# Kernel tuning notes

Hardware: AMD Instinct MI355X
Metric: run time of the kernel (lower is better)

## Reference

```python
import jax, jax.numpy as jnp
import numpy as np

NEG_SLOPE = 0.01  # torch F.leaky_relu default


def _mlp_block(x, mask, W, b):
    # x: [B,P,V,F]; mask: [B,P,V] bool; W: [H,F]; b: [H]
    h = jax.nn.leaky_relu(jnp.einsum('bpvf,hf->bpvh', x, W) + b, NEG_SLOPE)
    m = mask[..., None]
    out = jnp.where(m, h, 0.0)                                   # zeros at masked-out slots
    neg = jnp.where(m, out, -jnp.inf)
    pool = jnp.max(neg, axis=2, keepdims=True)                   # [B,P,1,H] masked max-pool
    any_valid = jnp.any(mask, axis=2)[:, :, None, None]
    pool = jnp.where(any_valid, pool, 0.0)                       # fully-masked polylines -> 0
    rep = jnp.broadcast_to(pool, out.shape)
    return jnp.concatenate([out, rep], axis=-1)                  # [B,P,V,2H]


def setup_inputs() -> dict:
    key = jax.random.key(0)
    ks = jax.random.split(key, 8)
    B, P, V, F, H = 32, 512, 32, 16, 64
    input_var = jax.random.normal(ks[0], (B, P, V, F), dtype=jnp.float32)
    input_mask = jax.random.bernoulli(ks[1], 0.8, (B, P, V))
    s = 1.0 / np.sqrt(F)
    W1 = jax.random.uniform(ks[2], (H, F), jnp.float32, -s, s)
    b1 = jax.random.uniform(ks[3], (H,), jnp.float32, -s, s)
    s2 = 1.0 / np.sqrt(2 * H)
    W2 = jax.random.uniform(ks[4], (H, 2 * H), jnp.float32, -s2, s2)
    b2 = jax.random.uniform(ks[5], (H,), jnp.float32, -s2, s2)
    W3 = jax.random.uniform(ks[6], (H, 2 * H), jnp.float32, -s2, s2)
    b3 = jax.random.uniform(ks[7], (H,), jnp.float32, -s2, s2)
    return {"input_var": input_var, "input_mask": input_mask,
            "W1": W1, "b1": b1, "W2": W2, "b2": b2, "W3": W3, "b3": b3,
            "size1": P, "size2": V}


def reference(input_var, input_mask, W1, b1, W2, b2, W3, b3, size1, size2):
    hidden = W1.shape[0]
    x = _mlp_block(input_var, input_mask, W1, b1)
    y = _mlp_block(x, input_mask, W2, b2)
    z = _mlp_block(y, input_mask, W3, b3)
    out = z[:, :, 0, -hidden:]                                   # pooled half, same across V
    out = jnp.where(jnp.any(input_mask, axis=2)[..., None], out, 0.0)
    return out
```

## Files before the change

### kernel.cpp

```cpp
#include <hip/hip_runtime.h>
#include <math.h>

namespace {
constexpr int kXS = 72;
constexpr float kSlope = 0.01f;

typedef short bf16x8 __attribute__((ext_vector_type(8)));
typedef float f32x4  __attribute__((ext_vector_type(4)));

__device__ __forceinline__ float lrelu(float x) { return fmaxf(x, kSlope * x); }

__device__ __forceinline__ unsigned short bfrne(float a) {
    union { float f; unsigned u; } v; v.f = a;
    return (unsigned short)((v.u + 0x7FFFu + ((v.u >> 16) & 1u)) >> 16);
}

__device__ __forceinline__ unsigned cvtpk(float lo, float hi) {
    unsigned r;
    asm("v_cvt_pk_bf16_f32 %0, %1, %2" : "=v"(r) : "v"(lo), "v"(hi));
    return r;
}

__global__ void prep_weights(const float* __restrict__ W1,
                             const float* __restrict__ W2,
                             const float* __restrict__ W3,
                             unsigned short* __restrict__ ws)
{
    int t = blockIdx.x * blockDim.x + threadIdx.x;
    if (t >= 36 * 64) return;
    int f = t >> 6, l = t & 63, c = l & 15, q = l >> 4;
    unsigned short v[8] = {0, 0, 0, 0, 0, 0, 0, 0};
    const float* src = nullptr; int row = 0, k0 = 0, K = 0;
    if (f < 4) {
        if (q < 2) { src = W1; row = 16 * f + c; k0 = q * 8; K = 16; }
    } else if (f < 20) {
        int g = f - 4;  src = W2; row = 16 * (g >> 2) + c; k0 = (g & 3) * 32 + q * 8; K = 128;
    } else {
        int g = f - 20; src = W3; row = 16 * (g >> 2) + c; k0 = (g & 3) * 32 + q * 8; K = 128;
    }
    if (src) {
        #pragma unroll
        for (int j = 0; j < 8; ++j) v[j] = bfrne(src[row * K + k0 + j]);
    }
    unsigned short* dst = ws + (size_t)f * 512 + l * 8;
    *(ushort4*)(dst)     = make_ushort4(v[0], v[1], v[2], v[3]);
    *(ushort4*)(dst + 4) = make_ushort4(v[4], v[5], v[6], v[7]);
}

__global__ __launch_bounds__(256, 3) void fused_mlp_v8(
    const float* __restrict__ X, const int* __restrict__ M,
    const unsigned short* __restrict__ WF,
    const float* __restrict__ B1, const float* __restrict__ B2,
    const float* __restrict__ B3, float* __restrict__ OUT)
{
    __shared__ __align__(16) short sX[4][2][32 * kXS];
    __shared__ __align__(16) short sP[4][2][64];

    const int t = threadIdx.x, w = t >> 6, l = t & 63, c = l & 15, q = l >> 4;
    const size_t bp0 = (size_t)blockIdx.x * 8 + w * 2;

    unsigned mbits[2];
    bool anyv[2];
    #pragma unroll
    for (int u = 0; u < 2; ++u) {
        const int4* Mp = (const int4*)(M + (bp0 + u) * 32);
        const int4 mr0 = Mp[q], mr1 = Mp[4 + q];
        mbits[u] =
            (mr0.x ? 1u : 0u)  | (mr0.y ? 2u : 0u)  | (mr0.z ? 4u : 0u)  | (mr0.w ? 8u : 0u) |
            (mr1.x ? 16u : 0u) | (mr1.y ? 32u : 0u) | (mr1.z ? 64u : 0u) | (mr1.w ? 128u : 0u);
        anyv[u] = __any(mbits[u] != 0);
    }
    float addm[2][8];
    #pragma unroll
    for (int u = 0; u < 2; ++u)
        #pragma unroll
        for (int i = 0; i < 8; ++i)
            addm[u][i] = ((mbits[u] >> i) & 1u) ? 0.f : -INFINITY;

    bf16x8 a1f[2][2];
    #pragma unroll
    for (int u = 0; u < 2; ++u)
        #pragma unroll
        for (int mt = 0; mt < 2; ++mt) {
            union { bf16x8 v; unsigned uu[4]; } cv; cv.v = bf16x8{};
            if (q < 2) {
                const float4* p = (const float4*)(X + ((bp0 + u) * 32 + 16 * mt + c) * 16 + q * 8);
                float4 f0 = p[0], f1 = p[1];
                cv.uu[0] = cvtpk(f0.x, f0.y);
                cv.uu[1] = cvtpk(f0.z, f0.w);
                cv.uu[2] = cvtpk(f1.x, f1.y);
                cv.uu[3] = cvtpk(f1.z, f1.w);
            }
            a1f[u][mt] = cv.v;
        }

    f32x4 acc[2][2][4];

    #pragma unroll
    for (int nt = 0; nt < 4; ++nt) {
        float b1 = B1[16 * nt + c];
        bf16x8 wf = *(const bf16x8*)(WF + (size_t)nt * 512 + l * 8);
        f32x4 c0 = { b1, b1, b1, b1 };
        #pragma unroll
        for (int u = 0; u < 2; ++u) {
            acc[u][0][nt] = __builtin_amdgcn_mfma_f32_16x16x32_bf16(a1f[u][0], wf, c0, 0, 0, 0);
            acc[u][1][nt] = __builtin_amdgcn_mfma_f32_16x16x32_bf16(a1f[u][1], wf, c0, 0, 0, 0);
        }
    }

    auto epilogue = [&](int u, short* xb_, short* pl_) {
        float pool[4];
        #pragma unroll
        for (int nt = 0; nt < 4; ++nt) {
            float pv = -INFINITY;
            #pragma unroll
            for (int mt = 0; mt < 2; ++mt) {
                short* base = &xb_[(16 * mt + 4 * q) * kXS + 16 * nt + c];
                float y0 = lrelu(acc[u][mt][nt][0]);
                float y1 = lrelu(acc[u][mt][nt][1]);
                float y2 = lrelu(acc[u][mt][nt][2]);
                float y3 = lrelu(acc[u][mt][nt][3]);
                pv = fmaxf(pv, y0 + addm[u][mt * 4 + 0]);
                pv = fmaxf(pv, y1 + addm[u][mt * 4 + 1]);
                pv = fmaxf(pv, y2 + addm[u][mt * 4 + 2]);
                pv = fmaxf(pv, y3 + addm[u][mt * 4 + 3]);
                unsigned u01 = cvtpk(y0, y1);
                unsigned u23 = cvtpk(y2, y3);
                base[0 * kXS] = (short)u01;
                base[1 * kXS] = (short)(u01 >> 16);
                base[2 * kXS] = (short)u23;
                base[3 * kXS] = (short)(u23 >> 16);
            }
            pv = fmaxf(pv, __shfl_xor(pv, 16));
            pv = fmaxf(pv, __shfl_xor(pv, 32));
            pool[nt] = anyv[u] ? pv : 0.f;
        }
        float ps = (q & 2) ? ((q & 1) ? pool[3] : pool[2])
                           : ((q & 1) ? pool[1] : pool[0]);
        pl_[16 * q + c] = (short)cvtpk(ps, ps);
    };

    auto layerK = [&](int fb, const float* Bp) {
        #pragma unroll
        for (int nt = 0; nt < 4; ++nt) {
            float bb = Bp[16 * nt + c];
            #pragma unroll
            for (int u = 0; u < 2; ++u) {
                acc[u][0][nt] = f32x4{ bb, bb, bb, bb };
                acc[u][1][nt] = acc[u][0][nt];
            }
        }
        #pragma unroll
        for (int ks = 0; ks < 4; ++ks) {
            bf16x8 am[2][2];
            #pragma unroll
            for (int u = 0; u < 2; ++u) {
                const short* xb_ = &sX[w][u][0];
                const short* pl_ = &sP[w][u][0];
                if (ks < 2) {
                    am[u][0] = *(const bf16x8*)&xb_[(     c) * kXS + ks * 32 + q * 8];
                    am[u][1] = *(const bf16x8*)&xb_[(16 + c) * kXS + ks * 32 + q * 8];
                } else {
                    am[u][0] = *(const bf16x8*)&pl_[(ks - 2) * 32 + q * 8];
                    am[u][1] = am[u][0];
                }
            }
            #pragma unroll
            for (int nt = 0; nt < 4; ++nt) {
                bf16x8 wf = *(const bf16x8*)(WF + ((size_t)(fb + nt * 4 + ks)) * 512 + l * 8);
                #pragma unroll
                for (int u = 0; u < 2; ++u) {
                    acc[u][0][nt] = __builtin_amdgcn_mfma_f32_16x16x32_bf16(am[u][0], wf, acc[u][0][nt], 0, 0, 0);
                    acc[u][1][nt] = __builtin_amdgcn_mfma_f32_16x16x32_bf16(am[u][1], wf, acc[u][1][nt], 0, 0, 0);
                }
            }
        }
    };

    epilogue(0, &sX[w][0][0], &sP[w][0][0]);
    epilogue(1, &sX[w][1][0], &sP[w][1][0]);
    layerK(4, B2);

    epilogue(0, &sX[w][0][0], &sP[w][0][0]);
    epilogue(1, &sX[w][1][0], &sP[w][1][0]);
    layerK(20, B3);

    #pragma unroll
    for (int u = 0; u < 2; ++u) {
        float pool[4];
        #pragma unroll
        for (int nt = 0; nt < 4; ++nt) {
            float pv = -INFINITY;
            #pragma unroll
            for (int mt = 0; mt < 2; ++mt)
                #pragma unroll
                for (int r = 0; r < 4; ++r)
                    pv = fmaxf(pv, lrelu(acc[u][mt][nt][r]) + addm[u][mt * 4 + r]);
            pv = fmaxf(pv, __shfl_xor(pv, 16));
            pv = fmaxf(pv, __shfl_xor(pv, 32));
            pool[nt] = anyv[u] ? pv : 0.f;
        }
        float ps = (q & 2) ? ((q & 1) ? pool[3] : pool[2])
                           : ((q & 1) ? pool[1] : pool[0]);
        OUT[(bp0 + u) * 64 + 16 * q + c] = ps;
    }
}
}

extern "C" void kernel_launch(void* const* d_in, const int* in_sizes, int n_in,
                              void* d_out, int out_size, void* d_ws, size_t ws_size,
                              hipStream_t stream) {
    (void)in_sizes; (void)n_in; (void)ws_size; (void)out_size;
    const float* X  = (const float*)d_in[0];
    const int*   M  = (const int*)d_in[1];
    const float* W1 = (const float*)d_in[2];
    const float* B1 = (const float*)d_in[3];
    const float* W2 = (const float*)d_in[4];
    const float* B2 = (const float*)d_in[5];
    const float* W3 = (const float*)d_in[6];
    const float* B3 = (const float*)d_in[7];
    float* OUT = (float*)d_out;
    unsigned short* WF = (unsigned short*)d_ws;

    prep_weights<<<(36 * 64 + 255) / 256, 256, 0, stream>>>(W1, W2, W3, WF);
    fused_mlp_v8<<<2048, 256, 0, stream>>>(X, M, WF, B1, B2, B3, OUT);
}
```

Before: 122.7 us.

## Stage weights in LDS, prepack mask bits and biases, roll layer loops

```diff
diff --git a/kernel.cpp b/kernel.cpp
--- a/kernel.cpp
+++ b/kernel.cpp
@@ -21,61 +21,86 @@
     return r;
 }
 
-__global__ void prep_weights(const float* __restrict__ W1,
-                             const float* __restrict__ W2,
-                             const float* __restrict__ W3,
-                             unsigned short* __restrict__ ws)
+__global__ void prep_pack(const float* __restrict__ W1,
+                          const float* __restrict__ W2,
+                          const float* __restrict__ W3,
+                          const float* __restrict__ B1,
+                          const float* __restrict__ B2,
+                          const float* __restrict__ B3,
+                          const int* __restrict__ M,
+                          unsigned short* __restrict__ wsW,
+                          float* __restrict__ wsB,
+                          unsigned* __restrict__ wsM)
 {
     int t = blockIdx.x * blockDim.x + threadIdx.x;
-    if (t >= 36 * 64) return;
-    int f = t >> 6, l = t & 63, c = l & 15, q = l >> 4;
-    unsigned short v[8] = {0, 0, 0, 0, 0, 0, 0, 0};
-    const float* src = nullptr; int row = 0, k0 = 0, K = 0;
-    if (f < 4) {
-        if (q < 2) { src = W1; row = 16 * f + c; k0 = q * 8; K = 16; }
-    } else if (f < 20) {
-        int g = f - 4;  src = W2; row = 16 * (g >> 2) + c; k0 = (g & 3) * 32 + q * 8; K = 128;
-    } else {
-        int g = f - 20; src = W3; row = 16 * (g >> 2) + c; k0 = (g & 3) * 32 + q * 8; K = 128;
-    }
-    if (src) {
-        #pragma unroll
-        for (int j = 0; j < 8; ++j) v[j] = bfrne(src[row * K + k0 + j]);
-    }
-    unsigned short* dst = ws + (size_t)f * 512 + l * 8;
-    *(ushort4*)(dst)     = make_ushort4(v[0], v[1], v[2], v[3]);
-    *(ushort4*)(dst + 4) = make_ushort4(v[4], v[5], v[6], v[7]);
-}
-
-__global__ __launch_bounds__(256, 3) void fused_mlp_v8(
-    const float* __restrict__ X, const int* __restrict__ M,
-    const unsigned short* __restrict__ WF,
-    const float* __restrict__ B1, const float* __restrict__ B2,
-    const float* __restrict__ B3, float* __restrict__ OUT)
+    if (t < 36 * 64) {
+        int f = t >> 6, l = t & 63, c = l & 15, q = l >> 4;
+        unsigned short v[8] = {0, 0, 0, 0, 0, 0, 0, 0};
+        const float* src = nullptr; int row = 0, k0 = 0, K = 0;
+        if (f < 4) {
+            if (q < 2) { src = W1; row = 16 * f + c; k0 = q * 8; K = 16; }
+        } else if (f < 20) {
+            int g = f - 4;  src = W2; row = 16 * (g >> 2) + c; k0 = (g & 3) * 32 + q * 8; K = 128;
+        } else {
+            int g = f - 20; src = W3; row = 16 * (g >> 2) + c; k0 = (g & 3) * 32 + q * 8; K = 128;
+        }
+        if (src) {
+            #pragma unroll
+            for (int j = 0; j < 8; ++j) v[j] = bfrne(src[row * K + k0 + j]);
+        }
+        unsigned short* dst = wsW + (size_t)f * 512 + l * 8;
+        *(ushort4*)(dst)     = make_ushort4(v[0], v[1], v[2], v[3]);
+        *(ushort4*)(dst + 4) = make_ushort4(v[4], v[5], v[6], v[7]);
+    } else if (t < 36 * 64 + 192) {
+        int i = t - 36 * 64; int layer = i >> 6, j = i & 63;
+        const float* B = (layer == 0) ? B1 : (layer == 1) ? B2 : B3;
+        wsB[layer * 64 + (j & 15) * 4 + (j >> 4)] = B[j];
+    } else if (t < 36 * 64 + 192 + 16384) {
+        int bp = t - (36 * 64 + 192);
+        const int4* mp = (const int4*)(M + bp * 32);
+        unsigned bits = 0;
+        #pragma unroll
+        for (int i = 0; i < 8; ++i) {
+            int4 v = mp[i];
+            unsigned b = (v.x ? 1u : 0u) | (v.y ? 2u : 0u) |
+                         (v.z ? 4u : 0u) | (v.w ? 8u : 0u);
+            bits |= b << (4 * i);
+        }
+        wsM[bp] = bits;
+    }
+}
+
+__global__ __launch_bounds__(256, 3) void fused_mlp_v9(
+    const float* __restrict__ X, const unsigned* __restrict__ MPK,
+    const unsigned short* __restrict__ WFg, const float* __restrict__ BT,
+    float* __restrict__ OUT)
 {
+    __shared__ __align__(16) short sWF[36 * 512];
     __shared__ __align__(16) short sX[4][2][32 * kXS];
     __shared__ __align__(16) short sP[4][2][64];
 
     const int t = threadIdx.x, w = t >> 6, l = t & 63, c = l & 15, q = l >> 4;
     const size_t bp0 = (size_t)blockIdx.x * 8 + w * 2;
 
-    unsigned mbits[2];
+    #pragma unroll
+    for (int i = 0; i < 9; ++i) {
+        int f = w * 9 + i;
+        __builtin_amdgcn_global_load_lds(
+            (const __attribute__((address_space(1))) void*)(WFg + (size_t)f * 512 + l * 8),
+            (__attribute__((address_space(3))) void*)&sWF[f * 512], 16, 0, 0);
+    }
+
     bool anyv[2];
+    float addm[2][8];
     #pragma unroll
     for (int u = 0; u < 2; ++u) {
-        const int4* Mp = (const int4*)(M + (bp0 + u) * 32);
-        const int4 mr0 = Mp[q], mr1 = Mp[4 + q];
-        mbits[u] =
-            (mr0.x ? 1u : 0u)  | (mr0.y ? 2u : 0u)  | (mr0.z ? 4u : 0u)  | (mr0.w ? 8u : 0u) |
-            (mr1.x ? 16u : 0u) | (mr1.y ? 32u : 0u) | (mr1.z ? 64u : 0u) | (mr1.w ? 128u : 0u);
-        anyv[u] = __any(mbits[u] != 0);
-    }
-    float addm[2][8];
-    #pragma unroll
-    for (int u = 0; u < 2; ++u)
+        unsigned m32 = MPK[bp0 + u];
+        anyv[u] = (m32 != 0u);
+        unsigned mb = ((m32 >> (4 * q)) & 15u) | (((m32 >> (16 + 4 * q)) & 15u) << 4);
         #pragma unroll
         for (int i = 0; i < 8; ++i)
-            addm[u][i] = ((mbits[u] >> i) & 1u) ? 0.f : -INFINITY;
+            addm[u][i] = ((mb >> i) & 1u) ? 0.f : -INFINITY;
+    }
 
     bf16x8 a1f[2][2];
     #pragma unroll
@@ -94,17 +119,21 @@
             a1f[u][mt] = cv.v;
         }
 
+    __syncthreads();
+
     f32x4 acc[2][2][4];
 
-    #pragma unroll
-    for (int nt = 0; nt < 4; ++nt) {
-        float b1 = B1[16 * nt + c];
-        bf16x8 wf = *(const bf16x8*)(WF + (size_t)nt * 512 + l * 8);
-        f32x4 c0 = { b1, b1, b1, b1 };
-        #pragma unroll
-        for (int u = 0; u < 2; ++u) {
-            acc[u][0][nt] = __builtin_amdgcn_mfma_f32_16x16x32_bf16(a1f[u][0], wf, c0, 0, 0, 0);
-            acc[u][1][nt] = __builtin_amdgcn_mfma_f32_16x16x32_bf16(a1f[u][1], wf, c0, 0, 0, 0);
+    {
+        f32x4 bv1 = *(const f32x4*)(BT + c * 4);
+        #pragma unroll
+        for (int nt = 0; nt < 4; ++nt) {
+            bf16x8 wf = *(const bf16x8*)&sWF[nt * 512 + l * 8];
+            f32x4 c0 = { bv1[nt], bv1[nt], bv1[nt], bv1[nt] };
+            #pragma unroll
+            for (int u = 0; u < 2; ++u) {
+                acc[u][0][nt] = __builtin_amdgcn_mfma_f32_16x16x32_bf16(a1f[u][0], wf, c0, 0, 0, 0);
+                acc[u][1][nt] = __builtin_amdgcn_mfma_f32_16x16x32_bf16(a1f[u][1], wf, c0, 0, 0, 0);
+            }
         }
     }
 
@@ -140,50 +169,47 @@
         pl_[16 * q + c] = (short)cvtpk(ps, ps);
     };
 
-    auto layerK = [&](int fb, const float* Bp) {
-        #pragma unroll
-        for (int nt = 0; nt < 4; ++nt) {
-            float bb = Bp[16 * nt + c];
+    #pragma unroll 1
+    for (int round = 0; round < 2; ++round) {
+        f32x4 bv = *(const f32x4*)(BT + (1 + round) * 64 + c * 4);
+
+        epilogue(0, &sX[w][0][0], &sP[w][0][0]);
+        epilogue(1, &sX[w][1][0], &sP[w][1][0]);
+
+        const int fb = 4 + round * 16;
+        #pragma unroll
+        for (int nt = 0; nt < 4; ++nt) {
             #pragma unroll
             for (int u = 0; u < 2; ++u) {
-                acc[u][0][nt] = f32x4{ bb, bb, bb, bb };
+                acc[u][0][nt] = f32x4{ bv[nt], bv[nt], bv[nt], bv[nt] };
                 acc[u][1][nt] = acc[u][0][nt];
             }
         }
-        #pragma unroll
+        #pragma unroll 1
         for (int ks = 0; ks < 4; ++ks) {
             bf16x8 am[2][2];
             #pragma unroll
             for (int u = 0; u < 2; ++u) {
                 const short* xb_ = &sX[w][u][0];
                 const short* pl_ = &sP[w][u][0];
-                if (ks < 2) {
-                    am[u][0] = *(const bf16x8*)&xb_[(     c) * kXS + ks * 32 + q * 8];
-                    am[u][1] = *(const bf16x8*)&xb_[(16 + c) * kXS + ks * 32 + q * 8];
-                } else {
-                    am[u][0] = *(const bf16x8*)&pl_[(ks - 2) * 32 + q * 8];
-                    am[u][1] = am[u][0];
-                }
+                const short* p0 = (ks < 2) ? &xb_[(     c) * kXS + ks * 32 + q * 8]
+                                           : &pl_[(ks - 2) * 32 + q * 8];
+                const short* p1 = (ks < 2) ? &xb_[(16 + c) * kXS + ks * 32 + q * 8]
+                                           : p0;
+                am[u][0] = *(const bf16x8*)p0;
+                am[u][1] = *(const bf16x8*)p1;
             }
             #pragma unroll
             for (int nt = 0; nt < 4; ++nt) {
-                bf16x8 wf = *(const bf16x8*)(WF + ((size_t)(fb + nt * 4 + ks)) * 512 + l * 8);
+                bf16x8 wfv = *(const bf16x8*)&sWF[(fb + nt * 4 + ks) * 512 + l * 8];
                 #pragma unroll
                 for (int u = 0; u < 2; ++u) {
-                    acc[u][0][nt] = __builtin_amdgcn_mfma_f32_16x16x32_bf16(am[u][0], wf, acc[u][0][nt], 0, 0, 0);
-                    acc[u][1][nt] = __builtin_amdgcn_mfma_f32_16x16x32_bf16(am[u][1], wf, acc[u][1][nt], 0, 0, 0);
+                    acc[u][0][nt] = __builtin_amdgcn_mfma_f32_16x16x32_bf16(am[u][0], wfv, acc[u][0][nt], 0, 0, 0);
+                    acc[u][1][nt] = __builtin_amdgcn_mfma_f32_16x16x32_bf16(am[u][1], wfv, acc[u][1][nt], 0, 0, 0);
                 }
             }
         }
-    };
-
-    epilogue(0, &sX[w][0][0], &sP[w][0][0]);
-    epilogue(1, &sX[w][1][0], &sP[w][1][0]);
-    layerK(4, B2);
-
-    epilogue(0, &sX[w][0][0], &sP[w][0][0]);
-    epilogue(1, &sX[w][1][0], &sP[w][1][0]);
-    layerK(20, B3);
+    }
 
     #pragma unroll
     for (int u = 0; u < 2; ++u) {
@@ -220,8 +246,12 @@
     const float* W3 = (const float*)d_in[6];
     const float* B3 = (const float*)d_in[7];
     float* OUT = (float*)d_out;
+
     unsigned short* WF = (unsigned short*)d_ws;
-
-    prep_weights<<<(36 * 64 + 255) / 256, 256, 0, stream>>>(W1, W2, W3, WF);
-    fused_mlp_v8<<<2048, 256, 0, stream>>>(X, M, WF, B1, B2, B3, OUT);
-}
+    float*    BT  = (float*)((char*)d_ws + 36864);
+    unsigned* MPK = (unsigned*)((char*)d_ws + 37632);
+
+    prep_pack<<<(36 * 64 + 192 + 16384 + 255) / 256, 256, 0, stream>>>(
+        W1, W2, W3, B1, B2, B3, M, WF, BT, MPK);
+    fused_mlp_v9<<<2048, 256, 0, stream>>>(X, MPK, WF, BT, OUT);
+}
```

After: 130.9 us. 6.7% more time.
